# Kernel tuning notes

Measured on AMD Instinct MI355X. Metric: run time of the kernel, lower is better.

## Reference

```python
import jax, jax.numpy as jnp
import numpy as np

B, D = 16384, 2048          # batch, input_dim
N_TOP, N_CLASS = 8, 16      # top labels, bottom labels per top (uniform, contiguous ids)

def setup_inputs() -> dict:
    key = jax.random.key(0)
    k1, k2, k3, k4, k5 = jax.random.split(key, 5)
    INIT = 0.2  # matches init_weight uniform(-0.2, 0.2)
    return {
        "features": jax.random.normal(k1, (B, D), dtype=jnp.float32),
        "top_W": jax.random.uniform(k2, (N_TOP, D), minval=-INIT, maxval=INIT, dtype=jnp.float32),
        "top_b": jax.random.uniform(k3, (N_TOP,), minval=-INIT, maxval=INIT, dtype=jnp.float32),
        "bottom_W": jax.random.uniform(k4, (N_TOP, D, N_CLASS), minval=-INIT, maxval=INIT, dtype=jnp.float32),
        "bottom_b": jax.random.uniform(k5, (N_TOP, N_CLASS), minval=-INIT, maxval=INIT, dtype=jnp.float32),
    }

def reference(features, top_W, top_b, bottom_W, bottom_b):
    # dropout p=0.0 -> identity
    # top gate: linear + sigmoid, (b, n_top)
    top_scores = jax.nn.sigmoid(features @ top_W.T + top_b)
    # all per-top-label expert linears as one batched GEMM: (b, n_top, n_class)
    bottom_logits = jnp.einsum('bd,tdc->btc', features, bottom_W) + bottom_b
    bottom_scores = jax.nn.softmax(bottom_logits, axis=-1)
    # scatter-combine: bottom ids of top i are contiguous [i*N_CLASS, (i+1)*N_CLASS),
    # so the column scatter is a reshape. (b, n_bottom_labels)
    final_scores = (top_scores[:, :, None] * bottom_scores).reshape(features.shape[0], N_TOP * N_CLASS)
    return final_scores
```

## Files before the change

kernel.cpp:

```cpp
#include <hip/hip_runtime.h>


#define D_DIM 2048
#define NTILE 9
#define M_ROWS 16

using f32x4 = float __attribute__((ext_vector_type(4)));
using half8 = _Float16 __attribute__((ext_vector_type(8)));
using fp16x2 = __fp16 __attribute__((ext_vector_type(2)));

__global__ void prep_weights(const float* __restrict__ topW,
                             const float* __restrict__ botW,
                             _Float16* __restrict__ S) {
    int idx = blockIdx.x * blockDim.x + threadIdx.x;
    if (idx >= 4 * 16 * NTILE * 64) return;
    int lane = idx & 63;
    int tmp  = idx >> 6;
    int nt   = tmp % NTILE;
    int wks  = tmp / NTILE;
    int n     = nt * 16 + (lane & 15);
    int kbase = wks * 32 + (lane >> 4) * 8;

    _Float16 v[8];
    #pragma unroll
    for (int j = 0; j < 8; j++) {
        int k = kbase + j;
        float x = 0.0f;
        if (n < 8) {
            x = topW[n * D_DIM + k];
        } else if (n < 136) {
            int t = (n - 8) >> 4, c = (n - 8) & 15;
            x = botW[(t * D_DIM + k) * 16 + c];
        }
        v[j] = (_Float16)x;
    }
    *(half8*)(S + (size_t)idx * 8) = *(half8*)v;
}

static __device__ __forceinline__ half8 pack_af(f32x4 a, f32x4 b) {
    fp16x2 p0 = __builtin_amdgcn_cvt_pkrtz(a[0], a[1]);
    fp16x2 p1 = __builtin_amdgcn_cvt_pkrtz(a[2], a[3]);
    fp16x2 p2 = __builtin_amdgcn_cvt_pkrtz(b[0], b[1]);
    fp16x2 p3 = __builtin_amdgcn_cvt_pkrtz(b[2], b[3]);
    half8 r;
    r[0] = (_Float16)p0[0]; r[1] = (_Float16)p0[1];
    r[2] = (_Float16)p1[0]; r[3] = (_Float16)p1[1];
    r[4] = (_Float16)p2[0]; r[5] = (_Float16)p2[1];
    r[6] = (_Float16)p3[0]; r[7] = (_Float16)p3[1];
    return r;
}

__global__ __launch_bounds__(256, 4) void hc_fused(
        const float* __restrict__ feat, const _Float16* __restrict__ Bsw,
        const float* __restrict__ top_b, const float* __restrict__ bot_b,
        float* __restrict__ out) {
    __shared__ float red[4][M_ROWS][148];

    const int tid  = threadIdx.x;
    const int lane = tid & 63, wave = tid >> 6;
    const int quad = lane >> 4, low = lane & 15;
    const size_t row0 = (size_t)blockIdx.x * M_ROWS;

    const float* A0 = feat + (row0 + low) * D_DIM + wave * 512 + quad * 8;
    const _Float16* Bp = Bsw + (size_t)wave * (16 * NTILE * 512) + lane * 8;

    f32x4 acc[NTILE];
    #pragma unroll
    for (int i = 0; i < NTILE; i++) acc[i] = (f32x4)0.0f;

    f32x4 aC0, aC1, aN0, aN1;
    aC0 = *(const f32x4*)(A0);
    aC1 = *(const f32x4*)(A0 + 4);

#define STEP(KS, AL0, AL1, NL0, NL1) do {                                  \
        const _Float16* Bn_ = Bp + (size_t)(KS) * NTILE * 512;             \
        half8 b0_ = *(const half8*)(Bn_);                                  \
        half8 b1_ = *(const half8*)(Bn_ + 1 * 512);                        \
        half8 b2_ = *(const half8*)(Bn_ + 2 * 512);                        \
        half8 b3_ = *(const half8*)(Bn_ + 3 * 512);                        \
        half8 b4_ = *(const half8*)(Bn_ + 4 * 512);                        \
        half8 b5_ = *(const half8*)(Bn_ + 5 * 512);                        \
        half8 b6_ = *(const half8*)(Bn_ + 6 * 512);                        \
        half8 b7_ = *(const half8*)(Bn_ + 7 * 512);                        \
        half8 b8_ = *(const half8*)(Bn_ + 8 * 512);                        \
        if ((KS) < 15) {                                                   \
            NL0 = *(const f32x4*)(A0 + ((KS) + 1) * 32);                   \
            NL1 = *(const f32x4*)(A0 + ((KS) + 1) * 32 + 4);               \
        }                                                                  \
        const half8 af_ = pack_af(AL0, AL1);                               \
        acc[0] = __builtin_amdgcn_mfma_f32_16x16x32_f16(af_, b0_, acc[0], 0, 0, 0); \
        acc[1] = __builtin_amdgcn_mfma_f32_16x16x32_f16(af_, b1_, acc[1], 0, 0, 0); \
        acc[2] = __builtin_amdgcn_mfma_f32_16x16x32_f16(af_, b2_, acc[2], 0, 0, 0); \
        acc[3] = __builtin_amdgcn_mfma_f32_16x16x32_f16(af_, b3_, acc[3], 0, 0, 0); \
        acc[4] = __builtin_amdgcn_mfma_f32_16x16x32_f16(af_, b4_, acc[4], 0, 0, 0); \
        acc[5] = __builtin_amdgcn_mfma_f32_16x16x32_f16(af_, b5_, acc[5], 0, 0, 0); \
        acc[6] = __builtin_amdgcn_mfma_f32_16x16x32_f16(af_, b6_, acc[6], 0, 0, 0); \
        acc[7] = __builtin_amdgcn_mfma_f32_16x16x32_f16(af_, b7_, acc[7], 0, 0, 0); \
        acc[8] = __builtin_amdgcn_mfma_f32_16x16x32_f16(af_, b8_, acc[8], 0, 0, 0); \
    } while (0)

    STEP( 0, aC0, aC1, aN0, aN1);
    STEP( 1, aN0, aN1, aC0, aC1);
    STEP( 2, aC0, aC1, aN0, aN1);
    STEP( 3, aN0, aN1, aC0, aC1);
    STEP( 4, aC0, aC1, aN0, aN1);
    STEP( 5, aN0, aN1, aC0, aC1);
    STEP( 6, aC0, aC1, aN0, aN1);
    STEP( 7, aN0, aN1, aC0, aC1);
    STEP( 8, aC0, aC1, aN0, aN1);
    STEP( 9, aN0, aN1, aC0, aC1);
    STEP(10, aC0, aC1, aN0, aN1);
    STEP(11, aN0, aN1, aC0, aC1);
    STEP(12, aC0, aC1, aN0, aN1);
    STEP(13, aN0, aN1, aC0, aC1);
    STEP(14, aC0, aC1, aN0, aN1);
    STEP(15, aN0, aN1, aC0, aC1);
#undef STEP

    #pragma unroll
    for (int nt = 0; nt < NTILE; nt++) {
        #pragma unroll
        for (int r = 0; r < 4; r++) {
            red[wave][quad * 4 + r][nt * 16 + low] = acc[nt][r];
        }
    }
    __syncthreads();

    if (tid < 128) {
        const int row = tid >> 3;
        const int top = tid & 7;

        float zt = top_b[top];
        #pragma unroll
        for (int w = 0; w < 4; w++) zt += red[w][row][top];
        const float sig = 1.0f / (1.0f + __expf(-zt));

        float z[16];
        float zmax = -1e30f;
        #pragma unroll
        for (int c = 0; c < 16; c++) {
            float v = bot_b[top * 16 + c];
            #pragma unroll
            for (int w = 0; w < 4; w++) v += red[w][row][8 + top * 16 + c];
            z[c] = v;
            zmax = fmaxf(zmax, v);
        }
        float s = 0.0f;
        #pragma unroll
        for (int c = 0; c < 16; c++) { z[c] = __expf(z[c] - zmax); s += z[c]; }
        const float scale = sig / s;

        float* o = out + (row0 + row) * 128 + top * 16;
        #pragma unroll
        for (int c = 0; c < 16; c += 4) {
            f32x4 v = { z[c] * scale, z[c+1] * scale, z[c+2] * scale, z[c+3] * scale };
            *(f32x4*)(o + c) = v;
        }
    }
}

extern "C" void kernel_launch(void* const* d_in, const int* in_sizes, int n_in,
                              void* d_out, int out_size, void* d_ws, size_t ws_size,
                              hipStream_t stream) {
    const float* feat  = (const float*)d_in[0];
    const float* topW  = (const float*)d_in[1];
    const float* topB  = (const float*)d_in[2];
    const float* botW  = (const float*)d_in[3];
    const float* botB  = (const float*)d_in[4];
    float* out = (float*)d_out;
    _Float16* Bsw = (_Float16*)d_ws;

    prep_weights<<<(4 * 16 * NTILE * 64 + 255) / 256, 256, 0, stream>>>(topW, botW, Bsw);
    hc_fused<<<16384 / M_ROWS, 256, 0, stream>>>(feat, Bsw, topB, botB, out);
}
```

Measured before the change: 226.5 us.

## Hand-schedule GEMM loads with inline-asm global loads and explicit vmcnt waits

Replaces the compiler-generated feature and weight loads in the main loop with inline-asm global_load_dwordx4 using a scalar base plus immediate offsets. A prefetch schedule keeps feature loads two K-steps ahead and issues the next weight tile right after each MFMA group. Explicit s_waitcnt vmcnt and sched_barrier calls pin the ordering. The aim is to overlap memory latency with MFMA work and cut address arithmetic, at the cost of fragile manual scheduling and losing the compiler's freedom to reorder.

```diff
diff --git a/kernel.cpp b/kernel.cpp
--- a/kernel.cpp
+++ b/kernel.cpp
@@ -50,6 +50,15 @@
     return r;
 }
 
+#define GL4(dst, voff, sbase, IMM)                                         \
+    asm volatile("global_load_dwordx4 %0, %1, %2 offset:%3"                \
+                 : "=v"(dst) : "v"(voff), "s"(sbase), "i"(IMM))
+
+#define VWAIT(N) do {                                                      \
+        asm volatile("s_waitcnt vmcnt(%0)" :: "i"(N) : "memory");          \
+        __builtin_amdgcn_sched_barrier(0);                                 \
+    } while (0)
+
 __global__ __launch_bounds__(256, 4) void hc_fused(
         const float* __restrict__ feat, const _Float16* __restrict__ Bsw,
         const float* __restrict__ top_b, const float* __restrict__ bot_b,
@@ -61,61 +70,69 @@
     const int quad = lane >> 4, low = lane & 15;
     const size_t row0 = (size_t)blockIdx.x * M_ROWS;
 
-    const float* A0 = feat + (row0 + low) * D_DIM + wave * 512 + quad * 8;
-    const _Float16* Bp = Bsw + (size_t)wave * (16 * NTILE * 512) + lane * 8;
+    const unsigned long long sA = (unsigned long long)feat;
+    const unsigned long long sB = (unsigned long long)Bsw;
+    const unsigned vAoff = (unsigned)(((row0 + low) * D_DIM + wave * 512 + quad * 8) * 4);
+    const unsigned vBoff = (unsigned)(wave * 147456 + lane * 16);
 
     f32x4 acc[NTILE];
     #pragma unroll
     for (int i = 0; i < NTILE; i++) acc[i] = (f32x4)0.0f;
 
-    f32x4 aC0, aC1, aN0, aN1;
-    aC0 = *(const f32x4*)(A0);
-    aC1 = *(const f32x4*)(A0 + 4);
+    f32x4 b0_, b1_, b2_, b3_, b4_, b5_, b6_, b7_, b8_;
+    f32x4 aX0, aX1, aY0, aY1;
 
-#define STEP(KS, AL0, AL1, NL0, NL1) do {                                  \
-        const _Float16* Bn_ = Bp + (size_t)(KS) * NTILE * 512;             \
-        half8 b0_ = *(const half8*)(Bn_);                                  \
-        half8 b1_ = *(const half8*)(Bn_ + 1 * 512);                        \
-        half8 b2_ = *(const half8*)(Bn_ + 2 * 512);                        \
-        half8 b3_ = *(const half8*)(Bn_ + 3 * 512);                        \
-        half8 b4_ = *(const half8*)(Bn_ + 4 * 512);                        \
-        half8 b5_ = *(const half8*)(Bn_ + 5 * 512);                        \
-        half8 b6_ = *(const half8*)(Bn_ + 6 * 512);                        \
-        half8 b7_ = *(const half8*)(Bn_ + 7 * 512);                        \
-        half8 b8_ = *(const half8*)(Bn_ + 8 * 512);                        \
-        if ((KS) < 15) {                                                   \
-            NL0 = *(const f32x4*)(A0 + ((KS) + 1) * 32);                   \
-            NL1 = *(const f32x4*)(A0 + ((KS) + 1) * 32 + 4);               \
-        }                                                                  \
-        const half8 af_ = pack_af(AL0, AL1);                               \
-        acc[0] = __builtin_amdgcn_mfma_f32_16x16x32_f16(af_, b0_, acc[0], 0, 0, 0); \
-        acc[1] = __builtin_amdgcn_mfma_f32_16x16x32_f16(af_, b1_, acc[1], 0, 0, 0); \
-        acc[2] = __builtin_amdgcn_mfma_f32_16x16x32_f16(af_, b2_, acc[2], 0, 0, 0); \
-        acc[3] = __builtin_amdgcn_mfma_f32_16x16x32_f16(af_, b3_, acc[3], 0, 0, 0); \
-        acc[4] = __builtin_amdgcn_mfma_f32_16x16x32_f16(af_, b4_, acc[4], 0, 0, 0); \
-        acc[5] = __builtin_amdgcn_mfma_f32_16x16x32_f16(af_, b5_, acc[5], 0, 0, 0); \
-        acc[6] = __builtin_amdgcn_mfma_f32_16x16x32_f16(af_, b6_, acc[6], 0, 0, 0); \
-        acc[7] = __builtin_amdgcn_mfma_f32_16x16x32_f16(af_, b7_, acc[7], 0, 0, 0); \
-        acc[8] = __builtin_amdgcn_mfma_f32_16x16x32_f16(af_, b8_, acc[8], 0, 0, 0); \
+#define ISSUE_B(KS) do {                                                   \
+        unsigned off_lo_ = vBoff + ((KS) * 9216 + 2048);                   \
+        unsigned off_hi_ = vBoff + ((KS) * 9216 + 6144);                   \
+        GL4(b0_, off_lo_, sB, -2048);                                      \
+        GL4(b1_, off_lo_, sB, -1024);                                      \
+        GL4(b2_, off_lo_, sB,     0);                                      \
+        GL4(b3_, off_lo_, sB,  1024);                                      \
+        GL4(b4_, off_hi_, sB, -2048);                                      \
+        GL4(b5_, off_hi_, sB, -1024);                                      \
+        GL4(b6_, off_hi_, sB,     0);                                      \
+        GL4(b7_, off_hi_, sB,  1024);                                      \
+        GL4(b8_, off_hi_, sB,  2048);                                      \
     } while (0)
 
-    STEP( 0, aC0, aC1, aN0, aN1);
-    STEP( 1, aN0, aN1, aC0, aC1);
-    STEP( 2, aC0, aC1, aN0, aN1);
-    STEP( 3, aN0, aN1, aC0, aC1);
-    STEP( 4, aC0, aC1, aN0, aN1);
-    STEP( 5, aN0, aN1, aC0, aC1);
-    STEP( 6, aC0, aC1, aN0, aN1);
-    STEP( 7, aN0, aN1, aC0, aC1);
-    STEP( 8, aC0, aC1, aN0, aN1);
-    STEP( 9, aN0, aN1, aC0, aC1);
-    STEP(10, aC0, aC1, aN0, aN1);
-    STEP(11, aN0, aN1, aC0, aC1);
-    STEP(12, aC0, aC1, aN0, aN1);
-    STEP(13, aN0, aN1, aC0, aC1);
-    STEP(14, aC0, aC1, aN0, aN1);
-    STEP(15, aN0, aN1, aC0, aC1);
-#undef STEP
+#define COMP(AL0, AL1) do {                                                \
+        const half8 af_ = pack_af(AL0, AL1);                               \
+        acc[0] = __builtin_amdgcn_mfma_f32_16x16x32_f16(af_, __builtin_bit_cast(half8, b0_), acc[0], 0, 0, 0); \
+        acc[1] = __builtin_amdgcn_mfma_f32_16x16x32_f16(af_, __builtin_bit_cast(half8, b1_), acc[1], 0, 0, 0); \
+        acc[2] = __builtin_amdgcn_mfma_f32_16x16x32_f16(af_, __builtin_bit_cast(half8, b2_), acc[2], 0, 0, 0); \
+        acc[3] = __builtin_amdgcn_mfma_f32_16x16x32_f16(af_, __builtin_bit_cast(half8, b3_), acc[3], 0, 0, 0); \
+        acc[4] = __builtin_amdgcn_mfma_f32_16x16x32_f16(af_, __builtin_bit_cast(half8, b4_), acc[4], 0, 0, 0); \
+        acc[5] = __builtin_amdgcn_mfma_f32_16x16x32_f16(af_, __builtin_bit_cast(half8, b5_), acc[5], 0, 0, 0); \
+        acc[6] = __builtin_amdgcn_mfma_f32_16x16x32_f16(af_, __builtin_bit_cast(half8, b6_), acc[6], 0, 0, 0); \
+        acc[7] = __builtin_amdgcn_mfma_f32_16x16x32_f16(af_, __builtin_bit_cast(half8, b7_), acc[7], 0, 0, 0); \
+        acc[8] = __builtin_amdgcn_mfma_f32_16x16x32_f16(af_, __builtin_bit_cast(half8, b8_), acc[8], 0, 0, 0); \
+        __builtin_amdgcn_sched_barrier(0);                                 \
+    } while (0)
+
+    ISSUE_B(0);
+    GL4(aX0, vAoff, sA,   0);  GL4(aX1, vAoff, sA,  16);
+    GL4(aY0, vAoff, sA, 128);  GL4(aY1, vAoff, sA, 144);
+
+    VWAIT(2); COMP(aX0, aX1); ISSUE_B( 1); GL4(aX0, vAoff, sA,  256); GL4(aX1, vAoff, sA,  272);
+    VWAIT(2); COMP(aY0, aY1); ISSUE_B( 2); GL4(aY0, vAoff, sA,  384); GL4(aY1, vAoff, sA,  400);
+    VWAIT(2); COMP(aX0, aX1); ISSUE_B( 3); GL4(aX0, vAoff, sA,  512); GL4(aX1, vAoff, sA,  528);
+    VWAIT(2); COMP(aY0, aY1); ISSUE_B( 4); GL4(aY0, vAoff, sA,  640); GL4(aY1, vAoff, sA,  656);
+    VWAIT(2); COMP(aX0, aX1); ISSUE_B( 5); GL4(aX0, vAoff, sA,  768); GL4(aX1, vAoff, sA,  784);
+    VWAIT(2); COMP(aY0, aY1); ISSUE_B( 6); GL4(aY0, vAoff, sA,  896); GL4(aY1, vAoff, sA,  912);
+    VWAIT(2); COMP(aX0, aX1); ISSUE_B( 7); GL4(aX0, vAoff, sA, 1024); GL4(aX1, vAoff, sA, 1040);
+    VWAIT(2); COMP(aY0, aY1); ISSUE_B( 8); GL4(aY0, vAoff, sA, 1152); GL4(aY1, vAoff, sA, 1168);
+    VWAIT(2); COMP(aX0, aX1); ISSUE_B( 9); GL4(aX0, vAoff, sA, 1280); GL4(aX1, vAoff, sA, 1296);
+    VWAIT(2); COMP(aY0, aY1); ISSUE_B(10); GL4(aY0, vAoff, sA, 1408); GL4(aY1, vAoff, sA, 1424);
+    VWAIT(2); COMP(aX0, aX1); ISSUE_B(11); GL4(aX0, vAoff, sA, 1536); GL4(aX1, vAoff, sA, 1552);
+    VWAIT(2); COMP(aY0, aY1); ISSUE_B(12); GL4(aY0, vAoff, sA, 1664); GL4(aY1, vAoff, sA, 1680);
+    VWAIT(2); COMP(aX0, aX1); ISSUE_B(13); GL4(aX0, vAoff, sA, 1792); GL4(aX1, vAoff, sA, 1808);
+    VWAIT(2); COMP(aY0, aY1); ISSUE_B(14); GL4(aY0, vAoff, sA, 1920); GL4(aY1, vAoff, sA, 1936);
+    VWAIT(2); COMP(aX0, aX1); ISSUE_B(15);
+    VWAIT(0); COMP(aY0, aY1);
+
+#undef ISSUE_B
+#undef COMP
 
     #pragma unroll
     for (int nt = 0; nt < NTILE; nt++) {
```

New measurement: 223.1 us. About the same (-1.5%).
